# Optimization experiments

Measured on AMD Instinct MI355X. Metric: run time of the kernel, lower is better.

## Reference

```python
import jax, jax.numpy as jnp
import numpy as np

B, H, S, D = 1, 2, 128, 64  # head_dim D = embed_dim // num_heads = 128 // 2


def setup_inputs() -> dict:
    key = jax.random.key(0)
    k1, k2, k3, k4, k5, k6 = jax.random.split(key, 6)
    scale1 = 1.0 / np.sqrt(2 * D)
    Q = jax.random.normal(k1, (B, H, S, D), dtype=jnp.float32)
    K = jax.random.normal(k2, (B, H, S, D), dtype=jnp.float32)
    # transport_net: Linear(2D -> 2D), Tanh, Linear(2D -> D*D)
    W1 = jax.random.uniform(k3, (2 * D, 2 * D), dtype=jnp.float32, minval=-scale1, maxval=scale1)
    b1 = jax.random.uniform(k4, (2 * D,), dtype=jnp.float32, minval=-scale1, maxval=scale1)
    W2 = jax.random.uniform(k5, (2 * D, D * D), dtype=jnp.float32, minval=-scale1, maxval=scale1)
    b2 = jax.random.uniform(k6, (D * D,), dtype=jnp.float32, minval=-scale1, maxval=scale1)
    return {"Q": Q, "K": K, "W1": W1, "b1": b1, "W2": W2, "b2": b2}


def reference(Q, K, W1, b1, W2, b2):
    b, h, s, d = Q.shape
    # Pairwise concat: combined[b,h,i,j] = [Q[b,h,i], K[b,h,j]]  -> [B,H,S,S,2D]
    Qe = jnp.broadcast_to(Q[:, :, :, None, :], (b, h, s, s, d))
    Ke = jnp.broadcast_to(K[:, :, None, :, :], (b, h, s, s, d))
    combined = jnp.concatenate([Qe, Ke], axis=-1)
    hidden = jnp.tanh(combined @ W1 + b1)                      # [B,H,S,S,2D]
    tm = (hidden @ W2 + b2).reshape(b, h, s, s, d, d)          # [B,H,S,S,D,D]
    # K_transported[b,h,i,j,:] = tm[b,h,i,j] @ K[b,h,j]
    Kt = jnp.einsum('bhijde,bhje->bhijd', tm, K)
    # mean over query index i (dim=2) -> [B,H,S,D]
    return Kt.mean(axis=2)
```

## Files before the change

### kernel.cpp

```cpp
#include <hip/hip_runtime.h>
#include <hip/hip_bf16.h>
#include <math.h>


#define H_ 2
#define S_ 128
#define D_ 64
#define C_ 128

__device__ __forceinline__ float ftanh(float x) {
    float e2 = __expf(2.0f * x);
    return 1.0f - 2.0f * __builtin_amdgcn_rcpf(e2 + 1.0f);
}

__global__ __launch_bounds__(128) void k1_ab(const float* __restrict__ Q,
                                             const float* __restrict__ K,
                                             const float* __restrict__ W1,
                                             float* __restrict__ A,
                                             float* __restrict__ Bm) {
    const int b = blockIdx.x;
    const int h = b >> 7;
    const int r = b & 127;
    const int c = threadIdx.x;

    __shared__ float qs[D_];
    __shared__ float ks[D_];
    if (c < 64)       qs[c]      = Q[h*S_*D_ + r*D_ + c];
    else              ks[c - 64] = K[h*S_*D_ + r*D_ + (c - 64)];
    __syncthreads();

    float a = 0.f, bb = 0.f;
#pragma unroll
    for (int d = 0; d < D_; ++d) {
        a  += qs[d] * W1[d*C_ + c];
        bb += ks[d] * W1[(64 + d)*C_ + c];
    }
    A[b*C_ + c]  = a;
    Bm[b*C_ + c] = bb;
}

__global__ __launch_bounds__(512) void k2_hbar(const float* __restrict__ A,
                                               const float* __restrict__ Bm,
                                               const float* __restrict__ b1,
                                               float* __restrict__ Hbar) {
    const int blk = blockIdx.x;
    const int h = blk >> 7;
    const int tid = threadIdx.x;
    const int c = tid & 127;
    const int q = tid >> 7;

    const float t = Bm[blk*C_ + c] + b1[c];
    const float* Ah = A + h*S_*C_ + q*32*C_;
    float acc = 0.f;
#pragma unroll 8
    for (int i = 0; i < 32; ++i) {
        acc += ftanh(Ah[i*C_ + c] + t);
    }

    __shared__ float red[512];
    red[tid] = acc;
    __syncthreads();
    if (q == 0) {
        Hbar[blk*C_ + c] = (red[c] + red[c + 128] + red[c + 256] + red[c + 384])
                           * (1.0f / (float)S_);
    }
}

__global__ __launch_bounds__(256) void k3_out(const float* __restrict__ K,
                                              const float* __restrict__ W2,
                                              const float* __restrict__ b2,
                                              const float* __restrict__ Hbar,
                                              float* __restrict__ out) {
    const int b = blockIdx.x;
    const int h  = b >> 7;
    const int d  = (b >> 1) & 63;
    const int jh = b & 1;
    const int lane = threadIdx.x & 63;
    const int w = __builtin_amdgcn_readfirstlane(threadIdx.x >> 6);
    const int jbase = jh*64 + w*16;

    float w2reg[C_];
#pragma unroll
    for (int c = 0; c < C_; ++c) {
        w2reg[c] = W2[c*4096 + d*64 + lane];
    }

    float kv[16];
#pragma unroll
    for (int jj = 0; jj < 16; ++jj) {
        kv[jj] = K[(h*S_ + jbase + jj)*D_ + lane];
    }
    const float b2v = b2[d*64 + lane];

    const float* __restrict__ Hbase = Hbar + (h*S_ + jbase)*C_;
    float acc[16];
#pragma unroll
    for (int jj = 0; jj < 16; ++jj) {
        const float* __restrict__ Hrow = Hbase + jj*C_;
        float t0 = 0.f, t1 = 0.f, t2 = 0.f, t3 = 0.f;
#pragma unroll
        for (int c = 0; c < C_; c += 4) {
            t0 += Hrow[c + 0] * w2reg[c + 0];
            t1 += Hrow[c + 1] * w2reg[c + 1];
            t2 += Hrow[c + 2] * w2reg[c + 2];
            t3 += Hrow[c + 3] * w2reg[c + 3];
        }
        acc[jj] = (t0 + t1) + (t2 + t3);
    }

#pragma unroll
    for (int jj = 0; jj < 16; ++jj) {
        float v = (acc[jj] + b2v) * kv[jj];
#pragma unroll
        for (int off = 32; off > 0; off >>= 1)
            v += __shfl_down(v, off);
        if (lane == 0)
            out[h*S_*D_ + (jbase + jj)*D_ + d] = v;
    }
}

extern "C" void kernel_launch(void* const* d_in, const int* in_sizes, int n_in,
                              void* d_out, int out_size, void* d_ws, size_t ws_size,
                              hipStream_t stream) {
    const float* Q  = (const float*)d_in[0];
    const float* K  = (const float*)d_in[1];
    const float* W1 = (const float*)d_in[2];
    const float* b1 = (const float*)d_in[3];
    const float* W2 = (const float*)d_in[4];
    const float* b2 = (const float*)d_in[5];
    float* out = (float*)d_out;

    float* A    = (float*)d_ws;
    float* Bm   = A  + H_*S_*C_;
    float* Hbar = Bm + H_*S_*C_;

    k1_ab  <<<H_*S_,   128, 0, stream>>>(Q, K, W1, A, Bm);
    k2_hbar<<<H_*S_,   512, 0, stream>>>(A, Bm, b1, Hbar);
    k3_out <<<H_*D_*2, 256, 0, stream>>>(K, W2, b2, Hbar, out);
}
```

Before: 97.40 us.

## Fuse W1 projection and tanh-mean into one kernel per hidden channel

```diff
diff --git a/kernel.cpp b/kernel.cpp
--- a/kernel.cpp
+++ b/kernel.cpp
@@ -13,56 +13,54 @@
     return 1.0f - 2.0f * __builtin_amdgcn_rcpf(e2 + 1.0f);
 }
 
-__global__ __launch_bounds__(128) void k1_ab(const float* __restrict__ Q,
-                                             const float* __restrict__ K,
-                                             const float* __restrict__ W1,
-                                             float* __restrict__ A,
-                                             float* __restrict__ Bm) {
+__global__ __launch_bounds__(256) void k12_hbar(const float* __restrict__ Q,
+                                                const float* __restrict__ K,
+                                                const float* __restrict__ W1,
+                                                const float* __restrict__ b1,
+                                                float* __restrict__ Hbar) {
     const int b = blockIdx.x;
     const int h = b >> 7;
-    const int r = b & 127;
-    const int c = threadIdx.x;
+    const int c = b & 127;
+    const int tid = threadIdx.x;
 
-    __shared__ float qs[D_];
-    __shared__ float ks[D_];
-    if (c < 64)       qs[c]      = Q[h*S_*D_ + r*D_ + c];
-    else              ks[c - 64] = K[h*S_*D_ + r*D_ + (c - 64)];
+    __shared__ float As[S_];
+    __shared__ float Bs[S_];
+    __shared__ float red[256];
+
+    {
+        const int r   = tid & 127;
+        const int sel = tid >> 7;
+        const float* __restrict__ src = sel ? K : Q;
+        const float* __restrict__ w1col = W1 + sel*64*C_ + c;
+        const float4* __restrict__ row = (const float4*)(src + (h*S_ + r)*D_);
+        float acc = 0.f;
+#pragma unroll
+        for (int d4 = 0; d4 < D_/4; ++d4) {
+            const float4 v = row[d4];
+            acc += v.x * w1col[(4*d4 + 0)*C_]
+                 + v.y * w1col[(4*d4 + 1)*C_]
+                 + v.z * w1col[(4*d4 + 2)*C_]
+                 + v.w * w1col[(4*d4 + 3)*C_];
+        }
+        if (sel == 0) As[r] = acc;
+        else          Bs[r] = acc + b1[c];
+    }
     __syncthreads();
 
-    float a = 0.f, bb = 0.f;
-#pragma unroll
-    for (int d = 0; d < D_; ++d) {
-        a  += qs[d] * W1[d*C_ + c];
-        bb += ks[d] * W1[(64 + d)*C_ + c];
+    {
+        const int j = tid & 127, q = tid >> 7;
+        const float t = Bs[j];
+        const float* __restrict__ Aq = As + q*64;
+        float acc = 0.f;
+#pragma unroll 8
+        for (int i = 0; i < 64; ++i)
+            acc += ftanh(Aq[i] + t);
+        red[tid] = acc;
     }
-    A[b*C_ + c]  = a;
-    Bm[b*C_ + c] = bb;
-}
+    __syncthreads();
 
-__global__ __launch_bounds__(512) void k2_hbar(const float* __restrict__ A,
-                                               const float* __restrict__ Bm,
-                                               const float* __restrict__ b1,
-                                               float* __restrict__ Hbar) {
-    const int blk = blockIdx.x;
-    const int h = blk >> 7;
-    const int tid = threadIdx.x;
-    const int c = tid & 127;
-    const int q = tid >> 7;
-
-    const float t = Bm[blk*C_ + c] + b1[c];
-    const float* Ah = A + h*S_*C_ + q*32*C_;
-    float acc = 0.f;
-#pragma unroll 8
-    for (int i = 0; i < 32; ++i) {
-        acc += ftanh(Ah[i*C_ + c] + t);
-    }
-
-    __shared__ float red[512];
-    red[tid] = acc;
-    __syncthreads();
-    if (q == 0) {
-        Hbar[blk*C_ + c] = (red[c] + red[c + 128] + red[c + 256] + red[c + 384])
-                           * (1.0f / (float)S_);
+    if (tid < 128) {
+        Hbar[(h*S_ + tid)*C_ + c] = (red[tid] + red[tid + 128]) * (1.0f/128.f);
     }
 }
 
@@ -130,11 +128,8 @@
     const float* b2 = (const float*)d_in[5];
     float* out = (float*)d_out;
 
-    float* A    = (float*)d_ws;
-    float* Bm   = A  + H_*S_*C_;
-    float* Hbar = Bm + H_*S_*C_;
+    float* Hbar = (float*)d_ws;
 
-    k1_ab  <<<H_*S_,   128, 0, stream>>>(Q, K, W1, A, Bm);
-    k2_hbar<<<H_*S_,   512, 0, stream>>>(A, Bm, b1, Hbar);
-    k3_out <<<H_*D_*2, 256, 0, stream>>>(K, W2, b2, Hbar, out);
+    k12_hbar<<<H_*S_,   256, 0, stream>>>(Q, K, W1, b1, Hbar);
+    k3_out  <<<H_*D_*2, 256, 0, stream>>>(K, W2, b2, Hbar, out);
 }
```

Measured after the change: 94.57 us. 1.03x faster.
